# Optimization experiments

Hardware: AMD Instinct MI355X
Metric: run time of the kernel (lower is better)

The kernel has to match this reference:

```python
import jax, jax.numpy as jnp
import numpy as np
import math

H = 512        # hidden_size (channels)
N = 64         # state_size
MAX_LEN = 4096 # kernel length L
BATCH = 8
SEQ = 4096     # seq len of input (== MAX_LEN here)


def _nplr(n):
    # HiPPO-LegS NPLR decomposition (done once at init, numpy float64 for eig stability)
    i = np.arange(n, dtype=np.float64)
    j = np.sqrt(2 * i + 1)
    A = -(np.tril(j[None, :] * j[:, None]) - np.diag(i))
    Bv = j.astype(np.complex128)
    p = j / np.sqrt(2.0)
    w, V = np.linalg.eig(A + p[None, :] * p[:, None])  # normal part; conj-pair eigvals adjacent
    w = w[::2].copy()          # [N/2]
    V = V[:, ::2].copy()       # [N, N/2]
    Bc = V.conj().T @ Bv       # [N/2]
    pc = V.conj().T @ p.astype(np.complex128)
    V_full = np.concatenate([V, V.conj()], axis=-1)      # [N, N]
    VtAV = V_full.conj().T @ A.astype(np.complex128) @ V_full  # [N, N]
    return w, pc, V, Bc, VtAV


def _ri(c):
    # complex -> trailing real/imag pair, float32 (mirrors torch.view_as_real)
    return np.stack([c.real, c.imag], axis=-1).astype(np.float32)


def setup_inputs() -> dict:
    rng = np.random.default_rng(0)
    w, p, V, Bc, Amat = _nplr(N)
    Brep = np.tile(Bc[None, :], (H, 1))                      # [H, N/2]
    C = rng.standard_normal((H, N)).astype(np.complex128)
    C = C @ V.conj()                                         # einsum('hn,nm->hm') -> [H, N/2]
    log_dt = math.log(1e-3) + (math.log(1e-1) - math.log(1e-3)) * rng.random(H)
    dt = np.exp(log_dt)[:, None, None]
    I = np.eye(N, dtype=np.complex128)[None]
    dA = np.linalg.inv(I - dt * Amat / 2) @ (I + dt * Amat / 2)   # [H, N, N]
    dA_power = I - np.linalg.matrix_power(dA, MAX_LEN)
    C2 = np.concatenate([C, C.conj()], axis=-1)              # [H, N]
    C2 = np.einsum('hmn,hm->hn', dA_power.conj(), C2)[:, : N // 2]
    p_rep = np.tile(p[None, None, :], (H, 1, 1))             # [H, 1, N/2]
    Bfull = np.concatenate([Brep[:, None, :], p_rep], axis=1)  # [H, 2, N/2]
    Cfull = np.concatenate([C2[:, None, :], p_rep], axis=1)    # [H, 2, N/2] (q == p)

    key = jax.random.key(0)
    kx, kd = jax.random.split(key)
    return {
        "x": jax.random.normal(kx, (BATCH, SEQ, H), dtype=jnp.float32),
        "log_dt": jnp.asarray(log_dt, dtype=jnp.float32),   # [H]
        "w_ri": jnp.asarray(_ri(w)),                        # [N/2, 2]
        "B_ri": jnp.asarray(_ri(Bfull)),                    # [H, 2, N/2, 2]
        "C_ri": jnp.asarray(_ri(Cfull)),                    # [H, 2, N/2, 2]
        "D": jax.random.normal(kd, (H,), dtype=jnp.float32),
    }


def _s4_kernel(log_dt, w_ri, B_ri, C_ri):
    L = MAX_LEN
    w = w_ri[..., 0] + 1j * w_ri[..., 1]   # [n] with n = N/2
    B = B_ri[..., 0] + 1j * B_ri[..., 1]   # [H, 2, n]
    C = C_ri[..., 0] + 1j * C_ri[..., 1]   # [H, 2, n]
    dt = jnp.exp(log_dt)                   # [H]
    freq = jnp.exp(-2j * jnp.pi / L * jnp.arange(L // 2 + 1))  # [F], F = L/2+1
    z = 2 * (1 - freq) / (1 + freq)        # bilinear-transformed frequencies

    v = C[:, :, None, :].conj() * B[:, None, :, :]   # [H, 2, 2, n]
    wd = w[None, :] * dt[:, None]                    # [H, n]
    # cauchy_mult: r = sum_n v/(z-w) + conj(v)/(z-conj(w)), as batched matmuls over n
    K1 = 1.0 / (z[None, None, :] - wd[:, :, None])          # [H, n, F]
    K2 = 1.0 / (z[None, None, :] - wd.conj()[:, :, None])   # [H, n, F]
    r = jnp.einsum('habn,hnf->habf', v, K1) + jnp.einsum('habn,hnf->habf', v.conj(), K2)
    r = r * dt[:, None, None, None]
    # Woodbury correction for the rank-1 (p, q) augmentation
    k_f = r[:, 0, 0, :] - r[:, 0, 1, :] * r[:, 1, 0, :] / (1 + r[:, 1, 1, :])  # [H, F]
    k_f = k_f * 2 / (1 + freq)
    return jnp.fft.irfft(k_f)   # [H, L]


def reference(x, log_dt, w_ri, B_ri, C_ri, D):
    k = _s4_kernel(log_dt, w_ri, B_ri, C_ri)     # [H, L]
    xt = jnp.transpose(x, (0, 2, 1))             # [B, H, Lx]
    L2 = 2 * MAX_LEN                              # conv pads to 2*kernel_len
    k_f = jnp.fft.rfft(k, n=L2)                  # [H, L2/2+1]
    x_f = jnp.fft.rfft(xt, n=L2)                 # [B, H, L2/2+1]
    y = jnp.fft.irfft(k_f[None] * x_f, n=L2)[..., : xt.shape[-1]]
    y = y + xt * D[None, :, None]                # skip connection
    return jnp.transpose(y, (0, 2, 1))           # [B, Lx, H]
```

## Files before the change

### kernel.cpp

```cpp
#include <hip/hip_runtime.h>
#include <math.h>

#define TPB 256
#define CTPB 1024
#define KTPB 512

__device__ __forceinline__ float2 cmul(float2 a, float2 b) {
    return make_float2(a.x * b.x - a.y * b.y, a.x * b.y + a.y * b.x);
}
__device__ __forceinline__ float2 cdivf(float2 a, float2 b) {
    float inv = 1.0f / (b.x * b.x + b.y * b.y);
    return make_float2((a.x * b.x + a.y * b.y) * inv, (a.y * b.x - a.x * b.y) * inv);
}
__device__ __forceinline__ float2 cadd(float2 a, float2 b) { return make_float2(a.x + b.x, a.y + b.y); }
__device__ __forceinline__ float2 csub(float2 a, float2 b) { return make_float2(a.x - b.x, a.y - b.y); }
__device__ __forceinline__ float2 mul_i(float2 a, float d) {
    return make_float2(-d * a.y, d * a.x);
}
__device__ __forceinline__ int brev11(int x) { return (int)(__brev((unsigned)x) >> 21); }
__device__ __forceinline__ int rev8(int x) {
    return ((x & 7) << 9) | (((x >> 3) & 7) << 6) | (((x >> 6) & 7) << 3) | ((x >> 9) & 7);
}
__device__ __forceinline__ int swz(int i) { return i ^ ((i >> 4) & 15) ^ ((i >> 8) & 15); }
__device__ __forceinline__ int swz13(int i) {
    return i ^ ((i >> 4) & 15) ^ ((i >> 8) & 15) ^ ((i >> 12) & 1);
}

__device__ __forceinline__ void dft8(const float2* x, float2* y, float d) {
    const float r = 0.70710678118f;
    float2 s0 = cadd(x[0], x[4]), t0 = csub(x[0], x[4]);
    float2 s1 = cadd(x[1], x[5]), t1 = csub(x[1], x[5]);
    float2 s2 = cadd(x[2], x[6]), t2 = csub(x[2], x[6]);
    float2 s3 = cadd(x[3], x[7]), t3 = csub(x[3], x[7]);
    t1 = cmul(t1, make_float2(r, d * r));
    t2 = mul_i(t2, d);
    t3 = cmul(t3, make_float2(-r, d * r));
    float2 u0 = cadd(s0, s2), v0 = csub(s0, s2);
    float2 u1 = cadd(s1, s3), v1 = mul_i(csub(s1, s3), d);
    y[0] = cadd(u0, u1); y[4] = csub(u0, u1);
    y[2] = cadd(v0, v1); y[6] = csub(v0, v1);
    float2 p0 = cadd(t0, t2), q0 = csub(t0, t2);
    float2 p1 = cadd(t1, t3), q1 = mul_i(csub(t1, t3), d);
    y[1] = cadd(p0, p1); y[5] = csub(p0, p1);
    y[3] = cadd(q0, q1); y[7] = csub(q0, q1);
}

__device__ __forceinline__ void dft8z(float2 x0, float2 x1, float2 x2, float2 x3,
                                      float2* y, float d) {
    const float r = 0.70710678118f;
    float2 u0 = cadd(x0, x2), v0 = csub(x0, x2);
    float2 u1 = cadd(x1, x3), v1 = mul_i(csub(x1, x3), d);
    float2 t1 = cmul(x1, make_float2(r, d * r));
    float2 t2 = mul_i(x2, d);
    float2 t3 = cmul(x3, make_float2(-r, d * r));
    float2 p0 = cadd(x0, t2), q0 = csub(x0, t2);
    float2 p1 = cadd(t1, t3), q1 = mul_i(csub(t1, t3), d);
    y[0] = cadd(u0, u1); y[4] = csub(u0, u1);
    y[2] = cadd(v0, v1); y[6] = csub(v0, v1);
    y[1] = cadd(p0, p1); y[5] = csub(p0, p1);
    y[3] = cadd(q0, q1); y[7] = csub(q0, q1);
}

__device__ __forceinline__ void dft8_lo(const float2* x, float2* y, float d) {
    const float r = 0.70710678118f;
    float2 s0 = cadd(x[0], x[4]), t0 = csub(x[0], x[4]);
    float2 s1 = cadd(x[1], x[5]), t1 = csub(x[1], x[5]);
    float2 s2 = cadd(x[2], x[6]), t2 = csub(x[2], x[6]);
    float2 s3 = cadd(x[3], x[7]), t3 = csub(x[3], x[7]);
    t1 = cmul(t1, make_float2(r, d * r));
    t2 = mul_i(t2, d);
    t3 = cmul(t3, make_float2(-r, d * r));
    float2 u0 = cadd(s0, s2), v0 = csub(s0, s2);
    float2 u1 = cadd(s1, s3), v1 = mul_i(csub(s1, s3), d);
    y[0] = cadd(u0, u1);
    y[2] = cadd(v0, v1);
    float2 p0 = cadd(t0, t2), q0 = csub(t0, t2);
    float2 p1 = cadd(t1, t3), q1 = mul_i(csub(t1, t3), d);
    y[1] = cadd(p0, p1);
    y[3] = cadd(q0, q1);
}

template <int HB, int DIR>
__device__ __forceinline__ void dif13(float2* s, int tid) {
    __syncthreads();
    const int h = 1 << HB;
    int j = tid & (h - 1);
    int base = ((tid >> HB) << (HB + 3)) + j;
    int s0 = swz13(base);
    float2 x[8];
#pragma unroll
    for (int k = 0; k < 8; ++k) x[k] = s[s0 ^ swz13(k << HB)];
    float2 y[8];
    dft8(x, y, (float)DIR);
    float ang = (float)DIR * 6.283185307179586f / (float)(h << 3) * (float)j;
    float c, sn;
    __sincosf(ang, &sn, &c);
    float2 w = make_float2(c, sn), wm = w;
    s[s0] = y[0];
#pragma unroll
    for (int m = 1; m < 8; ++m) {
        s[s0 ^ swz13(m << HB)] = cmul(wm, y[m]);
        wm = cmul(wm, w);
    }
}

template <int HB, int DIR>
__device__ __forceinline__ void dit13(float2* s, int tid) {
    __syncthreads();
    const int h = 1 << HB;
    int j = tid & (h - 1);
    int base = ((tid >> HB) << (HB + 3)) + j;
    int s0 = swz13(base);
    float ang = (float)DIR * 6.283185307179586f / (float)(h << 3) * (float)j;
    float c, sn;
    __sincosf(ang, &sn, &c);
    float2 w = make_float2(c, sn);
    float2 x[8];
    x[0] = s[s0];
    float2 wm = w;
#pragma unroll
    for (int k = 1; k < 8; ++k) {
        x[k] = cmul(wm, s[s0 ^ swz13(k << HB)]);
        wm = cmul(wm, w);
    }
    float2 y[8];
    dft8(x, y, (float)DIR);
#pragma unroll
    for (int m = 0; m < 8; ++m) s[s0 ^ swz13(m << HB)] = y[m];
}

template <int LOGN, int NT>
__device__ void fft8_dif(float2* s, int tid, float dir) {
    const int N = 1 << LOGN;
#pragma unroll
    for (int hb = LOGN - 3; hb >= 0; hb -= 3) {
        const int h = 1 << hb;
        const float astep = dir * 6.283185307179586f / (float)(h << 3);
        __syncthreads();
#pragma unroll
        for (int it = 0; it < (N >> 3) / NT; ++it) {
            const int b = tid + it * NT;
            int j = b & (h - 1);
            int base = ((b >> hb) << (hb + 3)) + j;
            int s0 = swz(base);
            float2 x[8];
#pragma unroll
            for (int k = 0; k < 8; ++k) x[k] = s[s0 ^ swz(k << hb)];
            float2 y[8];
            dft8(x, y, dir);
            if (hb != 0) {
                float ang = astep * (float)j;
                float c, sn;
                __sincosf(ang, &sn, &c);
                float2 w = make_float2(c, sn), wm = w;
                s[s0] = y[0];
#pragma unroll
                for (int m = 1; m < 8; ++m) {
                    s[s0 ^ swz(m << hb)] = cmul(wm, y[m]);
                    wm = cmul(wm, w);
                }
            } else {
#pragma unroll
                for (int m = 0; m < 8; ++m) s[s0 ^ swz(m << hb)] = y[m];
            }
        }
    }
    __syncthreads();
}

template <int LOGN, int NT>
__device__ void fft_dif2(float2* s, int tid, float dir) {
    const int N = 1 << LOGN;
    for (int st = LOGN - 1; st >= 0; --st) {
        __syncthreads();
        int half = 1 << st;
        for (int b = tid; b < (N >> 1); b += NT) {
            int j  = b & (half - 1);
            int i0 = ((b >> st) << (st + 1)) + j;
            int i1 = i0 + half;
            float2 u = s[i0], v = s[i1];
            float2 d = make_float2(u.x - v.x, u.y - v.y);
            s[i0] = make_float2(u.x + v.x, u.y + v.y);
            if (half > 1) {
                float ang = dir * 3.14159265358979f * (float)j / (float)half;
                float c, sn;
                __sincosf(ang, &sn, &c);
                s[i1] = cmul(make_float2(c, sn), d);
            } else {
                s[i1] = d;
            }
        }
    }
    __syncthreads();
}

__global__ __launch_bounds__(KTPB) void prep_kernel(
    const float* __restrict__ log_dt, const float* __restrict__ w_ri,
    const float* __restrict__ Bri, const float* __restrict__ Cri,
    const float* __restrict__ x, float2* __restrict__ Kt, float* __restrict__ xt) {
    __shared__ float2 s[4096];
    __shared__ float2 kf_last;
    __shared__ float2 wds[32];
    __shared__ float aab[4][32], rab[4][32];
    __shared__ float qn[32], pn[32];
    const int tid = threadIdx.x;

    if (blockIdx.x >= 512) {
        float* tile = (float*)s;
        const int tl_id = blockIdx.x - 512;
        const int b  = tl_id >> 9;
        const int rem = tl_id & 511;
        const int t0 = (rem >> 3) << 6;
        const int h0 = (rem & 7) << 6;
        const float4* xv = (const float4*)(x + ((size_t)b * 4096 + t0) * 512 + h0);
#pragma unroll
        for (int i = 0; i < 2; ++i) {
            int idx = tid + KTPB * i;
            int tl = idx >> 4, hq = idx & 15;
            float4 v = xv[(size_t)tl * 128 + hq];
            tile[tl * 65 + hq * 4 + 0] = v.x; tile[tl * 65 + hq * 4 + 1] = v.y;
            tile[tl * 65 + hq * 4 + 2] = v.z; tile[tl * 65 + hq * 4 + 3] = v.w;
        }
        __syncthreads();
        float* xo = xt + ((size_t)(b * 512 + h0)) * 4096 + t0;
#pragma unroll
        for (int i = 0; i < 2; ++i) {
            int idx = tid + KTPB * i;
            int hl = idx >> 4, tq = idx & 15;
            float4 v = make_float4(tile[(tq * 4 + 0) * 65 + hl], tile[(tq * 4 + 1) * 65 + hl],
                                   tile[(tq * 4 + 2) * 65 + hl], tile[(tq * 4 + 3) * 65 + hl]);
            ((float4*)(xo + (size_t)hl * 4096))[tq] = v;
        }
        return;
    }

    const int hh = blockIdx.x;
    float2* kfs = s + 2048;
    const float dt = expf(log_dt[hh]);
    if (tid < 32) {
        float wr = w_ri[2 * tid] * dt, wi = w_ri[2 * tid + 1] * dt;
        wds[tid] = make_float2(wr, wi);
        qn[tid]  = wr * wr + wi * wi;
        pn[tid]  = -2.0f * wr;
    }
    __syncthreads();
    if (tid < 128) {
        int a = tid >> 6, b = (tid >> 5) & 1, n = tid & 31;
        const float* Cp = Cri + (((hh * 2 + a) * 32) + n) * 2;
        const float* Bp = Bri + (((hh * 2 + b) * 32) + n) * 2;
        float Cr = Cp[0], Ci = Cp[1], Br = Bp[0], Bi = Bp[1];
        float2 v = make_float2(Cr * Br + Ci * Bi, Cr * Bi - Ci * Br);
        float2 wd = wds[n];
        aab[a * 2 + b][n] = -2.0f * (v.x * wd.x + v.y * wd.y);
        rab[a * 2 + b][n] = 2.0f * v.x;
    }
    __syncthreads();
    for (int f = tid; f < 2049; f += KTPB) {
        float th = (6.283185307179586f / 4096.0f) * (float)f;
        float cf = cosf(th), sf = sinf(th);
        float2 den = make_float2(1.0f + cf, -sf);
        float zt  = 2.0f * tanf(0.5f * th);
        float zt2 = zt * zt;
        float2 r00 = make_float2(0.f, 0.f), r01 = r00, r10 = r00, r11 = r00;
        for (int n = 0; n < 32; ++n) {
            float c   = qn[n] - zt2;
            float d   = pn[n] * zt;
            float inv = 1.0f / (c * c + d * d);
            float cc = c * inv, dd = d * inv;
            float a0 = aab[0][n], b0 = rab[0][n] * zt;
            r00.x += a0 * cc + b0 * dd; r00.y += b0 * cc - a0 * dd;
            float a1 = aab[1][n], b1 = rab[1][n] * zt;
            r01.x += a1 * cc + b1 * dd; r01.y += b1 * cc - a1 * dd;
            float a2 = aab[2][n], b2 = rab[2][n] * zt;
            r10.x += a2 * cc + b2 * dd; r10.y += b2 * cc - a2 * dd;
            float a3 = aab[3][n], b3 = rab[3][n] * zt;
            r11.x += a3 * cc + b3 * dd; r11.y += b3 * cc - a3 * dd;
        }
        r00.x *= dt; r00.y *= dt; r01.x *= dt; r01.y *= dt;
        r10.x *= dt; r10.y *= dt; r11.x *= dt; r11.y *= dt;
        float2 q  = cdivf(cmul(r01, r10), make_float2(1.0f + r11.x, r11.y));
        float2 k0 = make_float2(r00.x - q.x, r00.y - q.y);
        float2 kv = cmul(k0, cdivf(make_float2(2.0f, 0.0f), den));
        if (f < 2048) kfs[f] = kv; else kf_last = kv;
    }
    __syncthreads();

    for (int m = tid; m < 2048; m += KTPB) {
        float2 Xm = kfs[m];
        float2 Xc = (m == 0) ? kf_last : kfs[2048 - m];
        if (m == 0) { Xm.y = 0.0f; Xc.y = 0.0f; }
        float2 A  = make_float2(Xm.x + Xc.x, Xm.y - Xc.y);
        float2 Bv = make_float2(Xm.x - Xc.x, Xm.y + Xc.y);
        float ang = (3.14159265358979f / 2048.0f) * (float)m;
        float c, sn;
        __sincosf(ang, &sn, &c);
        float2 O = cmul(make_float2(c, sn), Bv);
        s[m] = make_float2(0.5f * (A.x - O.y), 0.5f * (A.y + O.x));
    }
    fft_dif2<11, KTPB>(s, tid, +1.0f);
    float2 reg[4];
    const float sc = 1.0f / 2048.0f;
#pragma unroll
    for (int i = 0; i < 4; ++i) {
        int t = tid + KTPB * i;
        float2 v = s[brev11(t)];
        reg[i] = make_float2(v.x * sc, v.y * sc);
    }
    __syncthreads();
#pragma unroll
    for (int i = 0; i < 4; ++i) {
        int t = tid + KTPB * i;
        s[swz(t)]        = reg[i];
        s[swz(t + 2048)] = make_float2(0.f, 0.f);
    }
    fft8_dif<12, KTPB>(s, tid, -1.0f);
    float2* K2 = Kt + ((size_t)hh << 13);
    const float isc = 1.0f / 8192.0f;
    const float2 Y0 = s[swz(0)];
    const float nyq = Y0.x - Y0.y;
    for (int q = tid; q < 8192; q += KTPB) {
        int j13 = ((q >> 10) & 7) | (((q >> 7) & 7) << 3) | (((q >> 4) & 7) << 6)
                | (((q >> 1) & 7) << 9) | ((q & 1) << 12);
        int cj = j13 > 4096;
        int j  = cj ? 8192 - j13 : j13;
        float2 X;
        if (j == 4096) {
            X = make_float2(nyq, 0.0f);
        } else {
            int p  = rev8(j);
            int pc = rev8((4096 - j) & 4095);
            float2 Yj = s[swz(p)], Yc = s[swz(pc)];
            float2 A  = make_float2(Yj.x + Yc.x, Yj.y - Yc.y);
            float2 Bv = make_float2(Yj.x - Yc.x, Yj.y + Yc.y);
            float ang = -(3.14159265358979f / 4096.0f) * (float)j;
            float c, sn;
            __sincosf(ang, &sn, &c);
            float2 t2 = cmul(make_float2(c, sn), make_float2(Bv.y, -Bv.x));
            X = make_float2(0.5f * (A.x + t2.x), 0.5f * (A.y + t2.y));
        }
        if (cj) X.y = -X.y;
        K2[q] = make_float2(X.x * isc, X.y * isc);
    }
}

__global__ __launch_bounds__(CTPB) void conv_kernel(const float* xt,
                                                    const float2* __restrict__ Kt,
                                                    const float* __restrict__ Dv,
                                                    float* yt) {
    __shared__ float2 s[8192];
    const int bp  = blockIdx.x >> 9;
    const int hch = blockIdx.x & 511;
    const int tid = threadIdx.x;
    const int stid = swz13(tid);
    float* r1 = (float*)(xt + ((size_t)(bp * 1024 + hch)) * 4096);
    float* r2 = r1 + (size_t)512 * 4096;

    {
        float2 z[4];
#pragma unroll
        for (int k = 0; k < 4; ++k) {
            int t = tid + (k << 10);
            z[k] = make_float2(r1[t], r2[t]);
        }
        float2 y[8];
        dft8z(z[0], z[1], z[2], z[3], y, -1.0f);
        float ang = -(6.283185307179586f / 8192.0f) * (float)tid;
        float c, sn;
        __sincosf(ang, &sn, &c);
        float2 w = make_float2(c, sn), wm = w;
        s[stid] = y[0];
#pragma unroll
        for (int m = 1; m < 8; ++m) {
            s[stid ^ swz13(m << 10)] = cmul(wm, y[m]);
            wm = cmul(wm, w);
        }
    }
    dif13<7, -1>(s, tid);
    dif13<4, -1>(s, tid);
    dif13<1, -1>(s, tid);
    __syncthreads();
#pragma unroll
    for (int it = 0; it < 4; ++it) {
        int b  = tid + (it << 10);
        int i0 = swz13(b << 1), i1 = swz13((b << 1) | 1);
        float2 u = s[i0], v = s[i1];
        s[i0] = cadd(u, v);
        s[i1] = csub(u, v);
    }
    __syncthreads();
    const float2* K = Kt + ((size_t)hch << 13);
#pragma unroll
    for (int i = 0; i < 8; ++i) {
        int p  = tid + (i << 10);
        int sp = stid ^ swz13(i << 10);
        s[sp] = cmul(s[sp], K[p]);
    }
    __syncthreads();
#pragma unroll
    for (int it = 0; it < 4; ++it) {
        int b  = tid + (it << 10);
        int i0 = swz13(b << 1), i1 = swz13((b << 1) | 1);
        float2 u = s[i0], v = s[i1];
        s[i0] = cadd(u, v);
        s[i1] = csub(u, v);
    }
    dit13<1, 1>(s, tid);
    dit13<4, 1>(s, tid);
    dit13<7, 1>(s, tid);
    __syncthreads();
    {
        float ang = (6.283185307179586f / 8192.0f) * (float)tid;
        float c, sn;
        __sincosf(ang, &sn, &c);
        float2 w = make_float2(c, sn);
        float2 x[8];
        x[0] = s[stid];
        float2 wm = w;
#pragma unroll
        for (int k = 1; k < 8; ++k) {
            x[k] = cmul(wm, s[stid ^ swz13(k << 10)]);
            wm = cmul(wm, w);
        }
        float2 y[4];
        dft8_lo(x, y, 1.0f);
        const float D = Dv[hch];
#pragma unroll
        for (int m = 0; m < 4; ++m) {
            int t = tid + (m << 10);
            float x1 = r1[t], x2 = r2[t];
            r1[t] = y[m].x + D * x1;
            r2[t] = y[m].y + D * x2;
        }
    }
}

__global__ __launch_bounds__(TPB) void transpose_out(const float* __restrict__ yt,
                                                     float* __restrict__ out) {
    __shared__ float tile[64][65];
    const int b = blockIdx.z, t0 = blockIdx.y * 64, h0 = blockIdx.x * 64;
    const int tid = threadIdx.x;
    const float* yp = yt + ((size_t)(b * 512 + h0)) * 4096 + t0;
#pragma unroll
    for (int i = 0; i < 4; ++i) {
        int idx = tid + TPB * i;
        int hl = idx >> 4, tq = idx & 15;
        float4 v = ((const float4*)(yp + (size_t)hl * 4096))[tq];
        tile[tq * 4 + 0][hl] = v.x; tile[tq * 4 + 1][hl] = v.y;
        tile[tq * 4 + 2][hl] = v.z; tile[tq * 4 + 3][hl] = v.w;
    }
    __syncthreads();
    float4* ov = (float4*)(out + ((size_t)b * 4096 + t0) * 512 + h0);
#pragma unroll
    for (int i = 0; i < 4; ++i) {
        int idx = tid + TPB * i;
        int tl = idx >> 4, hq = idx & 15;
        float4 v = make_float4(tile[tl][4 * hq + 0], tile[tl][4 * hq + 1],
                               tile[tl][4 * hq + 2], tile[tl][4 * hq + 3]);
        ov[(size_t)tl * 128 + hq] = v;
    }
}

extern "C" void kernel_launch(void* const* d_in, const int* in_sizes, int n_in,
                              void* d_out, int out_size, void* d_ws, size_t ws_size,
                              hipStream_t stream) {
    (void)in_sizes; (void)n_in; (void)out_size; (void)ws_size;
    const float* x      = (const float*)d_in[0];
    const float* log_dt = (const float*)d_in[1];
    const float* w_ri   = (const float*)d_in[2];
    const float* Bri    = (const float*)d_in[3];
    const float* Cri    = (const float*)d_in[4];
    const float* Dv     = (const float*)d_in[5];
    float* out = (float*)d_out;

    char* ws = (char*)d_ws;
    float*  xt = (float*)(ws);
    float2* Kt = (float2*)(ws + 67108864);

    prep_kernel<<<512 + 4096, KTPB, 0, stream>>>(log_dt, w_ri, Bri, Cri, x, Kt, xt);
    conv_kernel<<<2048, CTPB, 0, stream>>>(xt, Kt, Dv, xt);
    transpose_out<<<dim3(8, 64, 8), TPB, 0, stream>>>(xt, out);
}
```

Measured before the change: 293.9 us.

## Fuse final radix-2 butterflies with spectral multiply and precompute twiddle powers

The conv kernel's last forward radix-2 stage, the pointwise multiply by the kernel spectrum, and the first inverse radix-2 stage are merged into one pass. This removes two shared-memory round trips and two barriers. To support it, the kernel-generation stage now stores the spectrum as float4 pairs matching the butterfly pairing, so each pair loads with one vector read. The twiddle chains in dif13/dit13 are replaced with explicit powers, which shortens the serial dependency at the cost of a few extra multiplies.

After: 275.9 us. 1.07x faster.

```diff
diff --git a/kernel.cpp b/kernel.cpp
--- a/kernel.cpp
+++ b/kernel.cpp
@@ -95,13 +95,16 @@
     float ang = (float)DIR * 6.283185307179586f / (float)(h << 3) * (float)j;
     float c, sn;
     __sincosf(ang, &sn, &c);
-    float2 w = make_float2(c, sn), wm = w;
-    s[s0] = y[0];
-#pragma unroll
-    for (int m = 1; m < 8; ++m) {
-        s[s0 ^ swz13(m << HB)] = cmul(wm, y[m]);
-        wm = cmul(wm, w);
-    }
+    float2 w1 = make_float2(c, sn);
+    float2 w2 = cmul(w1, w1), w3 = cmul(w2, w1), w4 = cmul(w2, w2);
+    s[s0]                    = y[0];
+    s[s0 ^ swz13(1 << HB)]   = cmul(w1, y[1]);
+    s[s0 ^ swz13(2 << HB)]   = cmul(w2, y[2]);
+    s[s0 ^ swz13(3 << HB)]   = cmul(w3, y[3]);
+    s[s0 ^ swz13(4 << HB)]   = cmul(w4, y[4]);
+    s[s0 ^ swz13(5 << HB)]   = cmul(cmul(w4, w1), y[5]);
+    s[s0 ^ swz13(6 << HB)]   = cmul(cmul(w4, w2), y[6]);
+    s[s0 ^ swz13(7 << HB)]   = cmul(cmul(w4, w3), y[7]);
 }
 
 template <int HB, int DIR>
@@ -114,15 +117,17 @@
     float ang = (float)DIR * 6.283185307179586f / (float)(h << 3) * (float)j;
     float c, sn;
     __sincosf(ang, &sn, &c);
-    float2 w = make_float2(c, sn);
+    float2 w1 = make_float2(c, sn);
+    float2 w2 = cmul(w1, w1), w3 = cmul(w2, w1), w4 = cmul(w2, w2);
     float2 x[8];
     x[0] = s[s0];
-    float2 wm = w;
-#pragma unroll
-    for (int k = 1; k < 8; ++k) {
-        x[k] = cmul(wm, s[s0 ^ swz13(k << HB)]);
-        wm = cmul(wm, w);
-    }
+    x[1] = cmul(w1, s[s0 ^ swz13(1 << HB)]);
+    x[2] = cmul(w2, s[s0 ^ swz13(2 << HB)]);
+    x[3] = cmul(w3, s[s0 ^ swz13(3 << HB)]);
+    x[4] = cmul(w4, s[s0 ^ swz13(4 << HB)]);
+    x[5] = cmul(cmul(w4, w1), s[s0 ^ swz13(5 << HB)]);
+    x[6] = cmul(cmul(w4, w2), s[s0 ^ swz13(6 << HB)]);
+    x[7] = cmul(cmul(w4, w3), s[s0 ^ swz13(7 << HB)]);
     float2 y[8];
     dft8(x, y, (float)DIR);
 #pragma unroll
@@ -314,32 +319,26 @@
         s[swz(t + 2048)] = make_float2(0.f, 0.f);
     }
     fft8_dif<12, KTPB>(s, tid, -1.0f);
-    float2* K2 = Kt + ((size_t)hh << 13);
+    float4* K4 = (float4*)(Kt + ((size_t)hh << 13));
     const float isc = 1.0f / 8192.0f;
-    const float2 Y0 = s[swz(0)];
-    const float nyq = Y0.x - Y0.y;
-    for (int q = tid; q < 8192; q += KTPB) {
-        int j13 = ((q >> 10) & 7) | (((q >> 7) & 7) << 3) | (((q >> 4) & 7) << 6)
-                | (((q >> 1) & 7) << 9) | ((q & 1) << 12);
-        int cj = j13 > 4096;
-        int j  = cj ? 8192 - j13 : j13;
-        float2 X;
-        if (j == 4096) {
-            X = make_float2(nyq, 0.0f);
-        } else {
-            int p  = rev8(j);
-            int pc = rev8((4096 - j) & 4095);
-            float2 Yj = s[swz(p)], Yc = s[swz(pc)];
-            float2 A  = make_float2(Yj.x + Yc.x, Yj.y - Yc.y);
-            float2 Bv = make_float2(Yj.x - Yc.x, Yj.y + Yc.y);
-            float ang = -(3.14159265358979f / 4096.0f) * (float)j;
-            float c, sn;
-            __sincosf(ang, &sn, &c);
-            float2 t2 = cmul(make_float2(c, sn), make_float2(Bv.y, -Bv.x));
-            X = make_float2(0.5f * (A.x + t2.x), 0.5f * (A.y + t2.y));
-        }
-        if (cj) X.y = -X.y;
-        K2[q] = make_float2(X.x * isc, X.y * isc);
+    for (int i = 0; i < 8; ++i) {
+        int qh = tid + (i << 9);
+        int q  = qh << 1;
+        int j  = ((q >> 10) & 7) | (((q >> 7) & 7) << 3) | (((q >> 4) & 7) << 6)
+               | (((q >> 1) & 7) << 9);
+        int p  = rev8(j);
+        int pc = rev8((4096 - j) & 4095);
+        float2 Yj = s[swz(p)], Yc = s[swz(pc)];
+        float2 A  = make_float2(Yj.x + Yc.x, Yj.y - Yc.y);
+        float2 Bv = make_float2(Yj.x - Yc.x, Yj.y + Yc.y);
+        float ang = -(3.14159265358979f / 4096.0f) * (float)j;
+        float c, sn;
+        __sincosf(ang, &sn, &c);
+        float2 t2  = cmul(make_float2(c, sn), make_float2(Bv.y, -Bv.x));
+        float2 X   = make_float2(0.5f * (A.x + t2.x), 0.5f * (A.y + t2.y));
+        float2 t2c = cmul(make_float2(-c, sn), make_float2(Bv.y, Bv.x));
+        float2 Xc2 = make_float2(0.5f * (A.x + t2c.x), 0.5f * (-A.y + t2c.y));
+        K4[qh] = make_float4(X.x * isc, X.y * isc, Xc2.x * isc, -Xc2.y * isc);
     }
 }
 
@@ -379,30 +378,20 @@
     dif13<4, -1>(s, tid);
     dif13<1, -1>(s, tid);
     __syncthreads();
-#pragma unroll
-    for (int it = 0; it < 4; ++it) {
-        int b  = tid + (it << 10);
-        int i0 = swz13(b << 1), i1 = swz13((b << 1) | 1);
-        float2 u = s[i0], v = s[i1];
-        s[i0] = cadd(u, v);
-        s[i1] = csub(u, v);
-    }
-    __syncthreads();
-    const float2* K = Kt + ((size_t)hch << 13);
-#pragma unroll
-    for (int i = 0; i < 8; ++i) {
-        int p  = tid + (i << 10);
-        int sp = stid ^ swz13(i << 10);
-        s[sp] = cmul(s[sp], K[p]);
-    }
-    __syncthreads();
-#pragma unroll
-    for (int it = 0; it < 4; ++it) {
-        int b  = tid + (it << 10);
-        int i0 = swz13(b << 1), i1 = swz13((b << 1) | 1);
-        float2 u = s[i0], v = s[i1];
-        s[i0] = cadd(u, v);
-        s[i1] = csub(u, v);
+    {
+        const float4* K4 = (const float4*)(Kt + ((size_t)hch << 13));
+#pragma unroll
+        for (int it = 0; it < 4; ++it) {
+            int b  = tid + (it << 10);
+            int i0 = swz13(b << 1);
+            int i1 = i0 ^ 1;
+            float4 kk = K4[b];
+            float2 u = s[i0], v = s[i1];
+            float2 U = cmul(cadd(u, v), make_float2(kk.x, kk.y));
+            float2 V = cmul(csub(u, v), make_float2(kk.z, kk.w));
+            s[i0] = cadd(U, V);
+            s[i1] = csub(U, V);
+        }
     }
     dit13<1, 1>(s, tid);
     dit13<4, 1>(s, tid);
```
